# Performance work log

Measured on AMD Instinct MI355X. Metric: run time of the kernel, lower is better.

Reference implementation:

```python
import jax, jax.numpy as jnp
import numpy as np

K_HOPS = 10  # truncation order of the heat-kernel Taylor series


def setup_inputs() -> dict:
    key = jax.random.key(0)
    k1, k2, k3 = jax.random.split(key, 3)
    N, E, D_IN, D_OUT = 50000, 625000, 128, 128
    x = jax.random.normal(k1, (N, D_IN), dtype=jnp.float32)
    edge_index = jax.random.randint(k2, (2, E), 0, N, dtype=jnp.int64)
    t = jnp.asarray(5.0, dtype=jnp.float32)  # learnable diffusion time
    lim = 1.0 / np.sqrt(D_IN)
    W = jax.random.uniform(k3, (D_OUT, D_IN), dtype=jnp.float32, minval=-lim, maxval=lim)
    b = jnp.zeros((D_OUT,), dtype=jnp.float32)
    return {"x": x, "edge_index": edge_index, "t": t, "W": W, "b": b}


def reference(x, edge_index, t, W, b):
    N = x.shape[0]
    loop = jnp.arange(N, dtype=edge_index.dtype)
    src = jnp.concatenate([edge_index[0], loop])  # gcn_norm adds self-loops
    dst = jnp.concatenate([edge_index[1], loop])
    # symmetric normalization: norm_e = deg(dst)^-1/2 * deg(src)^-1/2
    deg = jnp.zeros((N,), dtype=x.dtype).at[dst].add(1.0)
    dinv = jnp.where(deg > 0, jax.lax.rsqrt(deg), 0.0)
    norm = dinv[src] * dinv[dst]  # [E+N]

    def prop(h):  # one hop of A_hat @ h via gather-scale-scatter
        msg = h[src] * norm[:, None]          # [E+N, D]
        return jax.ops.segment_sum(msg, dst, num_segments=N)

    # heat kernel: e^{-t} * sum_k t^k/k! * A_hat^k x
    coeff = jnp.exp(-t)
    out = coeff * x
    h = x
    for k in range(1, K_HOPS + 1):
        h = prop(h)
        coeff = coeff * t / k
        out = out + coeff * h
    return out @ W.T + b
```

## Files before the change

kernel.cpp:

```cpp
#include <hip/hip_runtime.h>
#include <math.h>

typedef float f4 __attribute__((ext_vector_type(4)));
typedef float f8 __attribute__((ext_vector_type(8)));
typedef _Float16 h8 __attribute__((ext_vector_type(8)));


__global__ void k_count(const int* __restrict__ dst, int* __restrict__ cnt, int E) {
  int e = blockIdx.x * blockDim.x + threadIdx.x;
  if (e < E) atomicAdd(&cnt[dst[e]], 1);
}

__global__ void k_scan_partial(const int* __restrict__ cnt, int* __restrict__ rowptr,
                               int* __restrict__ bsums, float* __restrict__ dinv, int N) {
  __shared__ int s[1024];
  int tid = threadIdx.x;
  int idx = blockIdx.x * 1024 + tid;
  int v = (idx < N) ? cnt[idx] : 0;
  if (idx < N) dinv[idx] = rsqrtf((float)(v + 1));
  int vp = (v + 3) & ~3;
  s[tid] = vp;
  __syncthreads();
  for (int off = 1; off < 1024; off <<= 1) {
    int add = (tid >= off) ? s[tid - off] : 0;
    __syncthreads();
    s[tid] += add;
    __syncthreads();
  }
  if (idx <= N) rowptr[idx] = s[tid] - vp;
  if (tid == 1023) bsums[blockIdx.x] = s[1023];
}

__global__ void k_scan_sums(int* __restrict__ bsums, int nb) {
  __shared__ int s[1024];
  int tid = threadIdx.x;
  int v = (tid < nb) ? bsums[tid] : 0;
  s[tid] = v;
  __syncthreads();
  for (int off = 1; off < 1024; off <<= 1) {
    int add = (tid >= off) ? s[tid - off] : 0;
    __syncthreads();
    s[tid] += add;
    __syncthreads();
  }
  if (tid < nb) bsums[tid] = s[tid] - v;
}

__global__ void k_add_offsets(int* __restrict__ rowptr, int* __restrict__ cursor,
                              const int* __restrict__ bsums, int N) {
  int idx = blockIdx.x * 1024 + threadIdx.x;
  if (idx <= N) {
    int v = rowptr[idx] + bsums[blockIdx.x];
    rowptr[idx] = v;
    if (idx < N) cursor[idx] = v;
  }
}

__global__ void k_scatter(const int* __restrict__ src, const int* __restrict__ dst,
                          const float* __restrict__ dinv, int* __restrict__ cursor,
                          int2* __restrict__ colw, int E) {
  int e = blockIdx.x * blockDim.x + threadIdx.x;
  if (e < E) {
    int s = src[e];
    int d = dst[e];
    int slot = atomicAdd(&cursor[d], 1);
    colw[slot] = make_int2(s, __float_as_int(dinv[s] * dinv[d]));
  }
}

__global__ void k_tohalf(const float* __restrict__ x, _Float16* __restrict__ xh, int total8) {
  int i = blockIdx.x * blockDim.x + threadIdx.x;
  if (i < total8) {
    f4 a = ((const f4*)x)[i * 2], b = ((const f4*)x)[i * 2 + 1];
    f8 v = {a.x, a.y, a.z, a.w, b.x, b.y, b.z, b.w};
    ((h8*)xh)[i] = __builtin_convertvector(v, h8);
  }
}

__global__ __launch_bounds__(256) void k_hop(
    const int* __restrict__ rowptr, const int2* __restrict__ colw,
    const float* __restrict__ dinv, const h8* __restrict__ xh,
    const h8* __restrict__ yin, h8* __restrict__ yout,
    const float* __restrict__ t_ptr, int j, int first, int N) {
  int wave = threadIdx.x >> 6;
  int lane = threadIdx.x & 63;
  int grp = lane >> 3;
  int r = (blockIdx.x * 4 + wave) * 4 + (grp >> 1);
  if (r >= N) return;
  int fl = (lane & 7) + (grp & 1) * 8;
  float t = t_ptr[0];
  float cj = expf(-t);
  for (int i = 1; i <= j; ++i) cj *= t / (float)i;
  float gs = first ? cj * t / (float)(j + 1) : 1.0f;

  auto G = [&](int idx) -> f8 {
    return __builtin_convertvector(yin[(size_t)idx * 16 + fl], f8);
  };

  f8 sA = {0,0,0,0,0,0,0,0}, sB = sA, sC = sA, sD = sA;
  int e = rowptr[r], end = rowptr[r + 1];
  for (; e < end; e += 4) {
    int4 p0 = *(const int4*)&colw[e];
    int4 p1 = *(const int4*)&colw[e + 2];
    sA += __int_as_float(p0.y) * G(p0.x);
    sB += __int_as_float(p0.w) * G(p0.z);
    sC += __int_as_float(p1.y) * G(p1.x);
    sD += __int_as_float(p1.w) * G(p1.z);
  }
  f8 s = (sA + sB) + (sC + sD);
  float di = dinv[r];
  s += (di * di) * G(r);
  f8 xr = __builtin_convertvector(xh[(size_t)r * 16 + fl], f8);
  s = gs * s + cj * xr;
  yout[(size_t)r * 16 + fl] = __builtin_convertvector(s, h8);
}

__global__ __launch_bounds__(256) void k_matmul(
    const h8* __restrict__ y16, const float* __restrict__ W,
    const float* __restrict__ bias, float* __restrict__ out, int N) {
  __shared__ h8 whiS[128 * 16];
  __shared__ h8 wloS[128 * 16];
  int tid = threadIdx.x;
  int rblk = blockIdx.x * 128;

#pragma unroll
  for (int it = 0; it < 8; ++it) {
    int idx = it * 256 + tid;
    int n = idx >> 4, g = idx & 15;
    f4 a = *(const f4*)&W[(size_t)n * 128 + g * 8];
    f4 b = *(const f4*)&W[(size_t)n * 128 + g * 8 + 4];
    f8 w = {a.x, a.y, a.z, a.w, b.x, b.y, b.z, b.w};
    h8 hi = __builtin_convertvector(w, h8);
    f8 hir = __builtin_convertvector(hi, f8);
    h8 lo = __builtin_convertvector(w - hir, h8);
    int slot = n * 16 + (g ^ (n & 7));
    whiS[slot] = hi;
    wloS[slot] = lo;
  }
  __syncthreads();

  int wave = tid >> 6, lane = tid & 63;
  int q = lane >> 4, fl = lane & 15;
  int rbase = rblk + wave * 32;

  f4 acc[2][8];
#pragma unroll
  for (int rt = 0; rt < 2; ++rt)
#pragma unroll
    for (int nt = 0; nt < 8; ++nt) acc[rt][nt] = (f4){0.f, 0.f, 0.f, 0.f};

#pragma unroll
  for (int s = 0; s < 4; ++s) {
    h8 aA, aB;
    {
      int r0 = rbase + fl;       if (r0 >= N) r0 = N - 1;
      int r1 = rbase + 16 + fl;  if (r1 >= N) r1 = N - 1;
      aA = y16[(size_t)r0 * 16 + s * 4 + q];
      aB = y16[(size_t)r1 * 16 + s * 4 + q];
    }
#pragma unroll
    for (int nt = 0; nt < 8; ++nt) {
      int n = nt * 16 + fl;
      int slot = n * 16 + ((s * 4 + q) ^ (n & 7));
      h8 bh = whiS[slot];
      h8 bl = wloS[slot];
      acc[0][nt] = __builtin_amdgcn_mfma_f32_16x16x32_f16(aA, bh, acc[0][nt], 0, 0, 0);
      acc[0][nt] = __builtin_amdgcn_mfma_f32_16x16x32_f16(aA, bl, acc[0][nt], 0, 0, 0);
      acc[1][nt] = __builtin_amdgcn_mfma_f32_16x16x32_f16(aB, bh, acc[1][nt], 0, 0, 0);
      acc[1][nt] = __builtin_amdgcn_mfma_f32_16x16x32_f16(aB, bl, acc[1][nt], 0, 0, 0);
    }
  }

#pragma unroll
  for (int rt = 0; rt < 2; ++rt) {
#pragma unroll
    for (int nt = 0; nt < 8; ++nt) {
      float bv = bias[nt * 16 + fl];
#pragma unroll
      for (int reg = 0; reg < 4; ++reg) {
        int r = rbase + rt * 16 + q * 4 + reg;
        if (r < N) out[(size_t)r * 128 + nt * 16 + fl] = acc[rt][nt][reg] + bv;
      }
    }
  }
}


extern "C" void kernel_launch(void* const* d_in, const int* in_sizes, int n_in,
                              void* d_out, int out_size, void* d_ws, size_t ws_size,
                              hipStream_t stream) {
  const float* x = (const float*)d_in[0];
  const int* ei = (const int*)d_in[1];
  const float* t = (const float*)d_in[2];
  const float* W = (const float*)d_in[3];
  const float* b = (const float*)d_in[4];
  int N = in_sizes[0] / 128;
  int E = in_sizes[1] / 2;
  const int* srcp = ei;
  const int* dstp = ei + E;
  float* out = (float*)d_out;

  char* ws = (char*)d_ws;
  size_t off = 0;
  auto alloc = [&](size_t bytes) -> void* {
    void* p = ws + off;
    off += (bytes + 255) & ~(size_t)255;
    return p;
  };
  h8*    yh0    = (h8*)alloc((size_t)N * 128 * 2);
  h8*    yh1    = (h8*)alloc((size_t)N * 128 * 2);
  h8*    xh     = (h8*)alloc((size_t)N * 128 * 2);
  int*   cnt    = (int*)alloc((size_t)N * 4);
  float* dinv   = (float*)alloc((size_t)N * 4);
  int*   rowptr = (int*)alloc((size_t)(N + 1) * 4);
  int*   cursor = (int*)alloc((size_t)N * 4);
  int*   bsums  = (int*)alloc(4096);
  size_t colw_bytes = ((size_t)E + 4 * (size_t)N) * 8;
  int2*  colw   = (int2*)alloc(colw_bytes);
  (void)ws_size;

  int nb_scan = (N + 1 + 1023) / 1024;

  hipMemsetAsync(cnt, 0, (size_t)N * 4, stream);
  hipMemsetAsync(colw, 0, colw_bytes, stream);
  k_count<<<(E + 255) / 256, 256, 0, stream>>>(dstp, cnt, E);
  k_scan_partial<<<nb_scan, 1024, 0, stream>>>(cnt, rowptr, bsums, dinv, N);
  k_scan_sums<<<1, 1024, 0, stream>>>(bsums, nb_scan);
  k_add_offsets<<<nb_scan, 1024, 0, stream>>>(rowptr, cursor, bsums, N);
  k_scatter<<<(E + 255) / 256, 256, 0, stream>>>(srcp, dstp, dinv, cursor, colw, E);
  k_tohalf<<<(N * 16 + 255) / 256, 256, 0, stream>>>(x, (_Float16*)xh, N * 16);

  int nblk = (N + 15) / 16;
  const h8* yin = xh;
  h8* bufs[2] = {yh0, yh1};
  for (int m = 0; m < 10; ++m) {
    h8* yout = bufs[m & 1];
    k_hop<<<nblk, 256, 0, stream>>>(rowptr, colw, dinv, xh, yin, yout,
                                    t, 9 - m, (m == 0) ? 1 : 0, N);
    yin = yout;
  }

  k_matmul<<<(N + 127) / 128, 256, 0, stream>>>(yin, W, b, out, N);
}
```

Before: 445.2 us.

## Sort rows by degree bucket to balance SpMM hop workload

Builds a permutation of rows grouped by in-degree through a small histogram, a scan and an atomic bucket placement. Each hop kernel then processes rows in that order, so the four rows sharing a wave have similar edge counts and divergence from uneven degrees drops. The cost is an extra indirection per row and scattered output writes, which weakens memory locality. Rows inside a bucket land in nondeterministic order because of the atomics.

Result: slower. 764.7 us (+71.8%).

```diff
diff --git a/kernel.cpp b/kernel.cpp
--- a/kernel.cpp
+++ b/kernel.cpp
@@ -5,6 +5,8 @@
 typedef float f8 __attribute__((ext_vector_type(8)));
 typedef _Float16 h8 __attribute__((ext_vector_type(8)));
 
+#define NB 64
+
 
 __global__ void k_count(const int* __restrict__ dst, int* __restrict__ cnt, int E) {
   int e = blockIdx.x * blockDim.x + threadIdx.x;
@@ -12,12 +14,17 @@
 }
 
 __global__ void k_scan_partial(const int* __restrict__ cnt, int* __restrict__ rowptr,
-                               int* __restrict__ bsums, float* __restrict__ dinv, int N) {
+                               int* __restrict__ bsums, float* __restrict__ dinv,
+                               int* __restrict__ hist, int N) {
   __shared__ int s[1024];
   int tid = threadIdx.x;
   int idx = blockIdx.x * 1024 + tid;
   int v = (idx < N) ? cnt[idx] : 0;
-  if (idx < N) dinv[idx] = rsqrtf((float)(v + 1));
+  if (idx < N) {
+    dinv[idx] = rsqrtf((float)(v + 1));
+    int b = v < (NB - 1) ? v : (NB - 1);
+    atomicAdd(&hist[b], 1);
+  }
   int vp = (v + 3) & ~3;
   s[tid] = vp;
   __syncthreads();
@@ -53,6 +60,28 @@
     int v = rowptr[idx] + bsums[blockIdx.x];
     rowptr[idx] = v;
     if (idx < N) cursor[idx] = v;
+  }
+}
+
+__global__ void k_binscan(const int* __restrict__ hist, int* __restrict__ bcur) {
+  int tid = threadIdx.x;
+  int v = hist[tid];
+  int sum = v;
+#pragma unroll
+  for (int off = 1; off < 64; off <<= 1) {
+    int o = __shfl_up(sum, off);
+    if (tid >= off) sum += o;
+  }
+  bcur[tid] = sum - v;
+}
+
+__global__ void k_permute(const int* __restrict__ cnt, int* __restrict__ bcur,
+                          int* __restrict__ perm, int N) {
+  int r = blockIdx.x * blockDim.x + threadIdx.x;
+  if (r < N) {
+    int v = cnt[r];
+    int b = v < (NB - 1) ? v : (NB - 1);
+    perm[atomicAdd(&bcur[b], 1)] = r;
   }
 }
 
@@ -79,14 +108,16 @@
 
 __global__ __launch_bounds__(256) void k_hop(
     const int* __restrict__ rowptr, const int2* __restrict__ colw,
-    const float* __restrict__ dinv, const h8* __restrict__ xh,
+    const float* __restrict__ dinv, const int* __restrict__ perm,
+    const h8* __restrict__ xh,
     const h8* __restrict__ yin, h8* __restrict__ yout,
     const float* __restrict__ t_ptr, int j, int first, int N) {
   int wave = threadIdx.x >> 6;
   int lane = threadIdx.x & 63;
   int grp = lane >> 3;
-  int r = (blockIdx.x * 4 + wave) * 4 + (grp >> 1);
-  if (r >= N) return;
+  int slot = (blockIdx.x * 4 + wave) * 4 + (grp >> 1);
+  if (slot >= N) return;
+  int r = perm[slot];
   int fl = (lane & 7) + (grp & 1) * 8;
   float t = t_ptr[0];
   float cj = expf(-t);
@@ -214,7 +245,10 @@
   float* dinv   = (float*)alloc((size_t)N * 4);
   int*   rowptr = (int*)alloc((size_t)(N + 1) * 4);
   int*   cursor = (int*)alloc((size_t)N * 4);
+  int*   perm   = (int*)alloc((size_t)N * 4);
   int*   bsums  = (int*)alloc(4096);
+  int*   hist   = (int*)alloc(NB * 4);
+  int*   bcur   = (int*)alloc(NB * 4);
   size_t colw_bytes = ((size_t)E + 4 * (size_t)N) * 8;
   int2*  colw   = (int2*)alloc(colw_bytes);
   (void)ws_size;
@@ -222,11 +256,14 @@
   int nb_scan = (N + 1 + 1023) / 1024;
 
   hipMemsetAsync(cnt, 0, (size_t)N * 4, stream);
+  hipMemsetAsync(hist, 0, NB * 4, stream);
   hipMemsetAsync(colw, 0, colw_bytes, stream);
   k_count<<<(E + 255) / 256, 256, 0, stream>>>(dstp, cnt, E);
-  k_scan_partial<<<nb_scan, 1024, 0, stream>>>(cnt, rowptr, bsums, dinv, N);
+  k_scan_partial<<<nb_scan, 1024, 0, stream>>>(cnt, rowptr, bsums, dinv, hist, N);
   k_scan_sums<<<1, 1024, 0, stream>>>(bsums, nb_scan);
   k_add_offsets<<<nb_scan, 1024, 0, stream>>>(rowptr, cursor, bsums, N);
+  k_binscan<<<1, 64, 0, stream>>>(hist, bcur);
+  k_permute<<<(N + 255) / 256, 256, 0, stream>>>(cnt, bcur, perm, N);
   k_scatter<<<(E + 255) / 256, 256, 0, stream>>>(srcp, dstp, dinv, cursor, colw, E);
   k_tohalf<<<(N * 16 + 255) / 256, 256, 0, stream>>>(x, (_Float16*)xh, N * 16);
 
@@ -235,7 +272,7 @@
   h8* bufs[2] = {yh0, yh1};
   for (int m = 0; m < 10; ++m) {
     h8* yout = bufs[m & 1];
-    k_hop<<<nblk, 256, 0, stream>>>(rowptr, colw, dinv, xh, yin, yout,
+    k_hop<<<nblk, 256, 0, stream>>>(rowptr, colw, dinv, perm, xh, yin, yout,
                                     t, 9 - m, (m == 0) ? 1 : 0, N);
     yin = yout;
   }
```
